# Optimization experiments

Measured on AMD Instinct MI355X. Metric: run time of the kernel, lower is better.

## Reference

```python
import jax, jax.numpy as jnp
import numpy as np
from jax import lax

DN = ('NCHW', 'OIHW', 'NCHW')
MAX_CLAMP = 0.75


def conv_s2(x, w):
    # kernel 9x9, stride 2, padding 4, no bias
    return lax.conv_general_dilated(x, w, window_strides=(2, 2),
                                    padding=[(4, 4), (4, 4)],
                                    dimension_numbers=DN)


def setup_inputs() -> dict:
    key = jax.random.key(0)
    k_x, k1, k2, k3, k4 = jax.random.split(key, 5)
    num_maps = 32
    x = jax.random.normal(k_x, (1024, 2, 128, 128), dtype=jnp.float32)
    # PyTorch Conv2d default init ~ U(-1/sqrt(fan_in), 1/sqrt(fan_in)); scale similarly
    w1 = jax.random.normal(k1, (8, 2, 9, 9), dtype=jnp.float32) * (1.0 / np.sqrt(2 * 81))
    w2 = jax.random.normal(k2, (8, 8, 9, 9), dtype=jnp.float32) * (1.0 / np.sqrt(8 * 81))
    w3 = jax.random.normal(k3, (num_maps, 8, 9, 9), dtype=jnp.float32) * (1.0 / np.sqrt(8 * 81))
    wfc = jax.random.normal(k4, (2, num_maps), dtype=jnp.float32) * (1.0 / np.sqrt(num_maps))
    return {"x": x, "w1": w1, "w2": w2, "w3": w3, "wfc": wfc}


def reference(x, w1, w2, w3, wfc):
    conv1 = jax.nn.relu(conv_s2(x, w1))                  # [B, 8, 64, 64]
    conv2 = jax.nn.relu(conv_s2(conv1, w2))              # [B, 8, 32, 32]
    conv3 = jax.nn.relu(conv_s2(conv2, w3))              # [B, M, 16, 16]
    # per-channel max over 16x16 spatial, threshold at 0.75*max, zero below
    maps_max = jnp.max(conv3, axis=(2, 3), keepdims=True) * MAX_CLAMP
    conv3_masked = jnp.where(conv3 < maps_max, 0.0, conv3)
    pool = jnp.mean(conv3_masked, axis=(2, 3))           # AvgPool2d((16,16)) -> [B, M]
    logits = pool @ wfc.T                                # Linear(M, 2, bias=False)
    y = jax.nn.log_softmax(logits, axis=1)
    return (y, conv3_masked, pool)
```

## Files before the change

### kernel.cpp

```cpp
#include <hip/hip_runtime.h>
#include <hip/hip_bf16.h>
#include <math.h>


#define RELU(v) fmaxf((v), 0.0f)

__device__ __forceinline__ int swzq(int q) { return q ^ ((q >> 3) & 7); }

__global__ __launch_bounds__(256) void conv1_kernel(
    const float* __restrict__ x, const float* __restrict__ w1,
    float* __restrict__ out1) {
  __shared__ float sIn[39 * 164];
  const int tid = threadIdx.x;
  const int b = blockIdx.x >> 2;
  const int oy0 = (blockIdx.x & 3) << 4;
  const int iy0 = 2 * oy0 - 4;
  const float* xb = x + (size_t)b * (2 * 128 * 128);

  const int ty = tid >> 4;
  const int tx = tid & 15;
  int roff[4];
#pragma unroll
  for (int q = 0; q < 4; q++) roff[q] = swzq(2 * tx + q) * 4;

  float acc[8][4];
#pragma unroll
  for (int co = 0; co < 8; co++)
#pragma unroll
    for (int i = 0; i < 4; i++) acc[co][i] = 0.f;

#pragma unroll 1
  for (int ci = 0; ci < 2; ci++) {
    __syncthreads();
    for (int i = tid; i < 39 * 34; i += 256) {
      int r = i / 34;
      int seg = i - r * 34;
      int gy = iy0 + r;
      float4 v = make_float4(0.f, 0.f, 0.f, 0.f);
      if (gy >= 0 && gy < 128 && seg >= 1 && seg <= 32)
        v = *reinterpret_cast<const float4*>(xb + (ci * 128 + gy) * 128 + (seg * 4 - 4));
      *reinterpret_cast<float4*>(&sIn[r * 164 + swzq(seg) * 4]) = v;
    }
    __syncthreads();
#pragma unroll 1
    for (int ky = 0; ky < 9; ky++) {
      const int rb = (2 * ty + ky) * 164;
      float xv[16];
#pragma unroll
      for (int q = 0; q < 4; q++) {
        float4 t = *reinterpret_cast<const float4*>(&sIn[rb + roff[q]]);
        xv[4 * q + 0] = t.x; xv[4 * q + 1] = t.y;
        xv[4 * q + 2] = t.z; xv[4 * q + 3] = t.w;
      }
#pragma unroll
      for (int co = 0; co < 8; co++) {
        const float* wr = w1 + (co * 2 + ci) * 81 + ky * 9;
        float w[9];
#pragma unroll
        for (int k = 0; k < 9; k++) w[k] = wr[k];
#pragma unroll
        for (int kx = 0; kx < 9; kx++)
#pragma unroll
          for (int i = 0; i < 4; i++)
            acc[co][i] = fmaf(xv[kx + 2 * i], w[kx], acc[co][i]);
      }
    }
  }
  const int oy = oy0 + ty;
  float* ob = out1 + (size_t)b * (8 * 64 * 64);
#pragma unroll
  for (int co = 0; co < 8; co++) {
    float4 v = make_float4(RELU(acc[co][0]), RELU(acc[co][1]),
                           RELU(acc[co][2]), RELU(acc[co][3]));
    *reinterpret_cast<float4*>(ob + (co * 64 + oy) * 64 + 4 * tx) = v;
  }
}

__global__ __launch_bounds__(256) void conv2_kernel(
    const float* __restrict__ in, const float* __restrict__ w2,
    float* __restrict__ out2) {
  __shared__ float sIn[71 * 84];
  const int tid = threadIdx.x;
  const int b = blockIdx.x;
  const float* ib = in + (size_t)b * (8 * 64 * 64);
  const int oy = tid >> 3;
  const int tx = tid & 7;
  int roff[4];
#pragma unroll
  for (int q = 0; q < 4; q++) roff[q] = swzq(2 * tx + q) * 4;

  float acc[8][4];
#pragma unroll
  for (int co = 0; co < 8; co++)
#pragma unroll
    for (int i = 0; i < 4; i++) acc[co][i] = 0.f;

#pragma unroll 1
  for (int ci = 0; ci < 8; ci++) {
    __syncthreads();
    for (int i = tid; i < 71 * 18; i += 256) {
      int r = i / 18;
      int seg = i - r * 18;
      int gy = r - 4;
      float4 v = make_float4(0.f, 0.f, 0.f, 0.f);
      if (gy >= 0 && gy < 64 && seg >= 1 && seg <= 16)
        v = *reinterpret_cast<const float4*>(ib + (ci * 64 + gy) * 64 + (seg * 4 - 4));
      *reinterpret_cast<float4*>(&sIn[r * 84 + swzq(seg) * 4]) = v;
    }
    __syncthreads();
#pragma unroll 1
    for (int ky = 0; ky < 9; ky++) {
      const int rb = (2 * oy + ky) * 84;
      float xv[16];
#pragma unroll
      for (int q = 0; q < 4; q++) {
        float4 t = *reinterpret_cast<const float4*>(&sIn[rb + roff[q]]);
        xv[4 * q + 0] = t.x; xv[4 * q + 1] = t.y;
        xv[4 * q + 2] = t.z; xv[4 * q + 3] = t.w;
      }
#pragma unroll
      for (int co = 0; co < 8; co++) {
        const float* wr = w2 + (co * 8 + ci) * 81 + ky * 9;
        float w[9];
#pragma unroll
        for (int k = 0; k < 9; k++) w[k] = wr[k];
#pragma unroll
        for (int kx = 0; kx < 9; kx++)
#pragma unroll
          for (int i = 0; i < 4; i++)
            acc[co][i] = fmaf(xv[kx + 2 * i], w[kx], acc[co][i]);
      }
    }
  }
  float* ob = out2 + (size_t)b * (8 * 32 * 32);
#pragma unroll
  for (int co = 0; co < 8; co++) {
    float4 v = make_float4(RELU(acc[co][0]), RELU(acc[co][1]),
                           RELU(acc[co][2]), RELU(acc[co][3]));
    *reinterpret_cast<float4*>(ob + (co * 32 + oy) * 32 + 4 * tx) = v;
  }
}

__global__ __launch_bounds__(256) void conv3_kernel(
    const float* __restrict__ in, const float* __restrict__ w3,
    float* __restrict__ masked_out, float* __restrict__ pool) {
  __shared__ float sIn[2 * 39 * 44];
  const int tid = threadIdx.x;
  const int b = blockIdx.x;
  const int co0 = __builtin_amdgcn_readfirstlane(tid >> 6) * 8;
  const int p = tid & 63;
  const int oy = p >> 2;
  const int oxg = p & 3;
  const float* ib = in + (size_t)b * (8 * 32 * 32);

  float acc[8][4];
#pragma unroll
  for (int co = 0; co < 8; co++)
#pragma unroll
    for (int i = 0; i < 4; i++) acc[co][i] = 0.f;

#pragma unroll 1
  for (int cg = 0; cg < 4; cg++) {
    __syncthreads();
    for (int i = tid; i < 2 * 39 * 10; i += 256) {
      int c = i / 390;
      int rem = i - c * 390;
      int r = rem / 10;
      int seg = rem - r * 10;
      int gy = r - 4;
      float4 v = make_float4(0.f, 0.f, 0.f, 0.f);
      if (gy >= 0 && gy < 32 && seg >= 1 && seg <= 8)
        v = *reinterpret_cast<const float4*>(ib + ((2 * cg + c) * 32 + gy) * 32 + (seg * 4 - 4));
      *reinterpret_cast<float4*>(&sIn[(c * 39 + r) * 44 + seg * 4]) = v;
    }
    __syncthreads();
#pragma unroll 1
    for (int c = 0; c < 2; c++) {
      const int ci = 2 * cg + c;
#pragma unroll 1
      for (int ky = 0; ky < 9; ky++) {
        const int rb = (c * 39 + 2 * oy + ky) * 44;
        float xv[16];
#pragma unroll
        for (int q = 0; q < 4; q++) {
          float4 t = *reinterpret_cast<const float4*>(&sIn[rb + (2 * oxg + q) * 4]);
          xv[4 * q + 0] = t.x; xv[4 * q + 1] = t.y;
          xv[4 * q + 2] = t.z; xv[4 * q + 3] = t.w;
        }
#pragma unroll
        for (int co = 0; co < 8; co++) {
          const float* wr = w3 + ((co0 + co) * 8 + ci) * 81 + ky * 9;
          float w[9];
#pragma unroll
          for (int k = 0; k < 9; k++) w[k] = wr[k];
#pragma unroll
          for (int kx = 0; kx < 9; kx++)
#pragma unroll
            for (int i = 0; i < 4; i++)
              acc[co][i] = fmaf(xv[kx + 2 * i], w[kx], acc[co][i]);
        }
      }
    }
  }

  float thr[8];
#pragma unroll
  for (int co = 0; co < 8; co++) {
#pragma unroll
    for (int i = 0; i < 4; i++) acc[co][i] = RELU(acc[co][i]);
    float m = fmaxf(fmaxf(acc[co][0], acc[co][1]), fmaxf(acc[co][2], acc[co][3]));
#pragma unroll
    for (int k = 32; k >= 1; k >>= 1) m = fmaxf(m, __shfl_xor(m, k));
    thr[co] = m * 0.75f;
  }

  float* mb = masked_out + ((size_t)b * 32 + co0) * 256 + 4 * p;
  float sum[8];
#pragma unroll
  for (int co = 0; co < 8; co++) {
    float4 v;
    v.x = (acc[co][0] < thr[co]) ? 0.f : acc[co][0];
    v.y = (acc[co][1] < thr[co]) ? 0.f : acc[co][1];
    v.z = (acc[co][2] < thr[co]) ? 0.f : acc[co][2];
    v.w = (acc[co][3] < thr[co]) ? 0.f : acc[co][3];
    *reinterpret_cast<float4*>(mb + co * 256) = v;
    float s = v.x + v.y + v.z + v.w;
#pragma unroll
    for (int k = 32; k >= 1; k >>= 1) s += __shfl_xor(s, k);
    sum[co] = s;
  }
  if (p == 0) {
#pragma unroll
    for (int co = 0; co < 8; co++)
      pool[(size_t)b * 32 + co0 + co] = sum[co] * (1.0f / 256.0f);
  }
}

__global__ __launch_bounds__(256) void head_kernel(
    const float* __restrict__ pool, const float* __restrict__ wfc,
    float* __restrict__ y) {
  __shared__ float sw[64];
  if (threadIdx.x < 64) sw[threadIdx.x] = wfc[threadIdx.x];
  __syncthreads();
  const int b = blockIdx.x * 256 + threadIdx.x;
  const float* pb = pool + (size_t)b * 32;
  float l0 = 0.f, l1 = 0.f;
#pragma unroll
  for (int q = 0; q < 8; q++) {
    float4 p = *reinterpret_cast<const float4*>(pb + 4 * q);
    l0 += p.x * sw[4 * q + 0] + p.y * sw[4 * q + 1] +
          p.z * sw[4 * q + 2] + p.w * sw[4 * q + 3];
    l1 += p.x * sw[32 + 4 * q + 0] + p.y * sw[32 + 4 * q + 1] +
          p.z * sw[32 + 4 * q + 2] + p.w * sw[32 + 4 * q + 3];
  }
  float m = fmaxf(l0, l1);
  float lz = logf(expf(l0 - m) + expf(l1 - m)) + m;
  float2 out = make_float2(l0 - lz, l1 - lz);
  *reinterpret_cast<float2*>(y + 2 * b) = out;
}

extern "C" void kernel_launch(void* const* d_in, const int* in_sizes, int n_in,
                              void* d_out, int out_size, void* d_ws, size_t ws_size,
                              hipStream_t stream) {
  const float* x   = (const float*)d_in[0];
  const float* w1  = (const float*)d_in[1];
  const float* w2  = (const float*)d_in[2];
  const float* w3  = (const float*)d_in[3];
  const float* wfc = (const float*)d_in[4];

  float* out = (float*)d_out;
  float* y      = out;
  float* masked = out + 2048;
  float* pool   = out + 2048 + 1024 * 32 * 256;

  float* c1 = (float*)d_ws;
  float* c2 = c1 + (size_t)1024 * 8 * 64 * 64;

  conv1_kernel<<<4096, 256, 0, stream>>>(x, w1, c1);
  conv2_kernel<<<1024, 256, 0, stream>>>(c1, w2, c2);
  conv3_kernel<<<1024, 256, 0, stream>>>(c2, w3, masked, pool);
  head_kernel<<<4, 256, 0, stream>>>(pool, wfc, y);
}
```

Baseline: 517.8 us.

## Prefetch conv tiles into registers, split conv2 blocks, fuse head into conv3

All three conv kernels now load the next input-channel tile from global memory into registers while computing the current one, then write it to shared memory, so load latency overlaps with FMA work. conv2 is split into two blocks per image, each with half the output rows and 2 outputs per thread, which doubles the grid and shrinks shared memory. conv3 pads rows to 64 floats with an XOR swizzle to avoid LDS bank conflicts, and absorbs the linear + log_softmax head, which removes one launch. The cost is more register pressure from the prefetch buffers, and conv2 now does less work per thread with more redundant weight loads.

```diff
diff --git a/kernel.cpp b/kernel.cpp
--- a/kernel.cpp
+++ b/kernel.cpp
@@ -29,19 +29,41 @@
 #pragma unroll
     for (int i = 0; i < 4; i++) acc[co][i] = 0.f;
 
-#pragma unroll 1
-  for (int ci = 0; ci < 2; ci++) {
-    __syncthreads();
-    for (int i = tid; i < 39 * 34; i += 256) {
-      int r = i / 34;
-      int seg = i - r * 34;
+  float4 pre[6];
+  auto issue = [&](int ci) {
+#pragma unroll
+    for (int k = 0; k < 5; k++) {
+      int idx = tid + 256 * k;
+      int r = idx >> 5, seg = idx & 31;
       int gy = iy0 + r;
       float4 v = make_float4(0.f, 0.f, 0.f, 0.f);
-      if (gy >= 0 && gy < 128 && seg >= 1 && seg <= 32)
+      if (idx < 1248 && gy >= 0 && gy < 128 && seg >= 1)
         v = *reinterpret_cast<const float4*>(xb + (ci * 128 + gy) * 128 + (seg * 4 - 4));
-      *reinterpret_cast<float4*>(&sIn[r * 164 + swzq(seg) * 4]) = v;
-    }
-    __syncthreads();
+      pre[k] = v;
+    }
+    {
+      int r = tid >> 1, seg = 32 + (tid & 1);
+      int gy = iy0 + r;
+      float4 v = make_float4(0.f, 0.f, 0.f, 0.f);
+      if (tid < 78 && gy >= 0 && gy < 128 && seg == 32)
+        v = *reinterpret_cast<const float4*>(xb + (ci * 128 + gy) * 128 + (seg * 4 - 4));
+      pre[5] = v;
+    }
+  };
+  auto wrlds = [&]() {
+#pragma unroll
+    for (int k = 0; k < 5; k++) {
+      int idx = tid + 256 * k;
+      int r = idx >> 5, seg = idx & 31;
+      if (idx < 1248)
+        *reinterpret_cast<float4*>(&sIn[r * 164 + swzq(seg) * 4]) = pre[k];
+    }
+    if (tid < 78) {
+      int r = tid >> 1, seg = 32 + (tid & 1);
+      *reinterpret_cast<float4*>(&sIn[r * 164 + swzq(seg) * 4]) = pre[5];
+    }
+  };
+  auto compute = [&](int ci) {
 #pragma unroll 1
     for (int ky = 0; ky < 9; ky++) {
       const int rb = (2 * ty + ky) * 164;
@@ -65,7 +87,14 @@
             acc[co][i] = fmaf(xv[kx + 2 * i], w[kx], acc[co][i]);
       }
     }
-  }
+  };
+
+  issue(0); wrlds(); __syncthreads();
+  issue(1);
+  compute(0);
+  __syncthreads(); wrlds(); __syncthreads();
+  compute(1);
+
   const int oy = oy0 + ty;
   float* ob = out1 + (size_t)b * (8 * 64 * 64);
 #pragma unroll
@@ -79,41 +108,63 @@
 __global__ __launch_bounds__(256) void conv2_kernel(
     const float* __restrict__ in, const float* __restrict__ w2,
     float* __restrict__ out2) {
-  __shared__ float sIn[71 * 84];
+  __shared__ float sIn[39 * 84];
   const int tid = threadIdx.x;
-  const int b = blockIdx.x;
+  const int b = blockIdx.x >> 1;
+  const int oy0 = (blockIdx.x & 1) << 4;
+  const int gy0 = 2 * oy0 - 4;
   const float* ib = in + (size_t)b * (8 * 64 * 64);
-  const int oy = tid >> 3;
-  const int tx = tid & 7;
-  int roff[4];
-#pragma unroll
-  for (int q = 0; q < 4; q++) roff[q] = swzq(2 * tx + q) * 4;
-
-  float acc[8][4];
-#pragma unroll
-  for (int co = 0; co < 8; co++)
-#pragma unroll
-    for (int i = 0; i < 4; i++) acc[co][i] = 0.f;
-
-#pragma unroll 1
-  for (int ci = 0; ci < 8; ci++) {
-    __syncthreads();
-    for (int i = tid; i < 71 * 18; i += 256) {
-      int r = i / 18;
-      int seg = i - r * 18;
-      int gy = r - 4;
-      float4 v = make_float4(0.f, 0.f, 0.f, 0.f);
-      if (gy >= 0 && gy < 64 && seg >= 1 && seg <= 16)
+  const int oy = tid >> 4;
+  const int tx = tid & 15;
+  int roff[3];
+#pragma unroll
+  for (int q = 0; q < 3; q++) roff[q] = swzq(tx + q) * 4;
+
+  float acc[8][2];
+#pragma unroll
+  for (int co = 0; co < 8; co++) { acc[co][0] = 0.f; acc[co][1] = 0.f; }
+
+  float4 pre[4];
+  auto issue = [&](int ci) {
+#pragma unroll
+    for (int k = 0; k < 3; k++) {
+      int idx = tid + 256 * k;
+      int r = idx >> 4, seg = idx & 15;
+      int gy = gy0 + r;
+      float4 v = make_float4(0.f, 0.f, 0.f, 0.f);
+      if (idx < 624 && gy >= 0 && gy < 64 && seg >= 1)
         v = *reinterpret_cast<const float4*>(ib + (ci * 64 + gy) * 64 + (seg * 4 - 4));
-      *reinterpret_cast<float4*>(&sIn[r * 84 + swzq(seg) * 4]) = v;
-    }
-    __syncthreads();
+      pre[k] = v;
+    }
+    {
+      int r = tid >> 1, seg = 16 + (tid & 1);
+      int gy = gy0 + r;
+      float4 v = make_float4(0.f, 0.f, 0.f, 0.f);
+      if (tid < 78 && gy >= 0 && gy < 64 && seg == 16)
+        v = *reinterpret_cast<const float4*>(ib + (ci * 64 + gy) * 64 + (seg * 4 - 4));
+      pre[3] = v;
+    }
+  };
+  auto wrlds = [&]() {
+#pragma unroll
+    for (int k = 0; k < 3; k++) {
+      int idx = tid + 256 * k;
+      int r = idx >> 4, seg = idx & 15;
+      if (idx < 624)
+        *reinterpret_cast<float4*>(&sIn[r * 84 + swzq(seg) * 4]) = pre[k];
+    }
+    if (tid < 78) {
+      int r = tid >> 1, seg = 16 + (tid & 1);
+      *reinterpret_cast<float4*>(&sIn[r * 84 + swzq(seg) * 4]) = pre[3];
+    }
+  };
+  auto compute = [&](int ci) {
 #pragma unroll 1
     for (int ky = 0; ky < 9; ky++) {
       const int rb = (2 * oy + ky) * 84;
-      float xv[16];
-#pragma unroll
-      for (int q = 0; q < 4; q++) {
+      float xv[12];
+#pragma unroll
+      for (int q = 0; q < 3; q++) {
         float4 t = *reinterpret_cast<const float4*>(&sIn[rb + roff[q]]);
         xv[4 * q + 0] = t.x; xv[4 * q + 1] = t.y;
         xv[4 * q + 2] = t.z; xv[4 * q + 3] = t.w;
@@ -125,26 +176,38 @@
 #pragma unroll
         for (int k = 0; k < 9; k++) w[k] = wr[k];
 #pragma unroll
-        for (int kx = 0; kx < 9; kx++)
-#pragma unroll
-          for (int i = 0; i < 4; i++)
-            acc[co][i] = fmaf(xv[kx + 2 * i], w[kx], acc[co][i]);
-      }
-    }
-  }
+        for (int kx = 0; kx < 9; kx++) {
+          acc[co][0] = fmaf(xv[kx], w[kx], acc[co][0]);
+          acc[co][1] = fmaf(xv[kx + 2], w[kx], acc[co][1]);
+        }
+      }
+    }
+  };
+
+  issue(0); wrlds(); __syncthreads();
+#pragma unroll 1
+  for (int ci = 0; ci < 8; ci++) {
+    if (ci < 7) issue(ci + 1);
+    compute(ci);
+    __syncthreads();
+    if (ci < 7) { wrlds(); __syncthreads(); }
+  }
+
   float* ob = out2 + (size_t)b * (8 * 32 * 32);
+  const int oyg = oy0 + oy;
 #pragma unroll
   for (int co = 0; co < 8; co++) {
-    float4 v = make_float4(RELU(acc[co][0]), RELU(acc[co][1]),
-                           RELU(acc[co][2]), RELU(acc[co][3]));
-    *reinterpret_cast<float4*>(ob + (co * 32 + oy) * 32 + 4 * tx) = v;
+    float2 v = make_float2(RELU(acc[co][0]), RELU(acc[co][1]));
+    *reinterpret_cast<float2*>(ob + (co * 32 + oyg) * 32 + 2 * tx) = v;
   }
 }
 
 __global__ __launch_bounds__(256) void conv3_kernel(
     const float* __restrict__ in, const float* __restrict__ w3,
-    float* __restrict__ masked_out, float* __restrict__ pool) {
-  __shared__ float sIn[2 * 39 * 44];
+    const float* __restrict__ wfc, float* __restrict__ masked_out,
+    float* __restrict__ pool, float* __restrict__ y) {
+  __shared__ float sIn[2 * 39 * 64];
+  __shared__ float sPool[32];
   const int tid = threadIdx.x;
   const int b = blockIdx.x;
   const int co0 = __builtin_amdgcn_readfirstlane(tid >> 6) * 8;
@@ -159,31 +222,61 @@
 #pragma unroll
     for (int i = 0; i < 4; i++) acc[co][i] = 0.f;
 
-#pragma unroll 1
-  for (int cg = 0; cg < 4; cg++) {
-    __syncthreads();
-    for (int i = tid; i < 2 * 39 * 10; i += 256) {
-      int c = i / 390;
-      int rem = i - c * 390;
-      int r = rem / 10;
-      int seg = rem - r * 10;
+  float4 pre[4];
+  auto issue = [&](int cg) {
+#pragma unroll
+    for (int k = 0; k < 3; k++) {
+      int idx = tid + 256 * k;
+      int cr = idx >> 3, seg = idx & 7;
+      int c = (cr >= 39) ? 1 : 0;
+      int r = cr - 39 * c;
       int gy = r - 4;
       float4 v = make_float4(0.f, 0.f, 0.f, 0.f);
-      if (gy >= 0 && gy < 32 && seg >= 1 && seg <= 8)
+      if (idx < 624 && gy >= 0 && gy < 32 && seg >= 1)
         v = *reinterpret_cast<const float4*>(ib + ((2 * cg + c) * 32 + gy) * 32 + (seg * 4 - 4));
-      *reinterpret_cast<float4*>(&sIn[(c * 39 + r) * 44 + seg * 4]) = v;
-    }
-    __syncthreads();
+      pre[k] = v;
+    }
+    {
+      int cr = tid >> 1, seg = 8 + (tid & 1);
+      int c = (cr >= 39) ? 1 : 0;
+      int r = cr - 39 * c;
+      int gy = r - 4;
+      float4 v = make_float4(0.f, 0.f, 0.f, 0.f);
+      if (tid < 156 && gy >= 0 && gy < 32 && seg == 8)
+        v = *reinterpret_cast<const float4*>(ib + ((2 * cg + c) * 32 + gy) * 32 + (seg * 4 - 4));
+      pre[3] = v;
+    }
+  };
+  auto wrlds = [&]() {
+#pragma unroll
+    for (int k = 0; k < 3; k++) {
+      int idx = tid + 256 * k;
+      int cr = idx >> 3, seg = idx & 7;
+      if (idx < 624) {
+        int slot = seg ^ ((cr >> 1) & 7);
+        *reinterpret_cast<float4*>(&sIn[cr * 64 + slot * 4]) = pre[k];
+      }
+    }
+    if (tid < 156) {
+      int cr = tid >> 1, seg = 8 + (tid & 1);
+      int slot = seg ^ ((cr >> 1) & 7);
+      *reinterpret_cast<float4*>(&sIn[cr * 64 + slot * 4]) = pre[3];
+    }
+  };
+  auto compute = [&](int cg) {
 #pragma unroll 1
     for (int c = 0; c < 2; c++) {
       const int ci = 2 * cg + c;
 #pragma unroll 1
       for (int ky = 0; ky < 9; ky++) {
-        const int rb = (c * 39 + 2 * oy + ky) * 44;
+        const int row = c * 39 + 2 * oy + ky;
+        const int rb = row * 64;
+        const int key = (row >> 1) & 7;
         float xv[16];
 #pragma unroll
         for (int q = 0; q < 4; q++) {
-          float4 t = *reinterpret_cast<const float4*>(&sIn[rb + (2 * oxg + q) * 4]);
+          int slot = (2 * oxg + q) ^ key;
+          float4 t = *reinterpret_cast<const float4*>(&sIn[rb + slot * 4]);
           xv[4 * q + 0] = t.x; xv[4 * q + 1] = t.y;
           xv[4 * q + 2] = t.z; xv[4 * q + 3] = t.w;
         }
@@ -201,6 +294,15 @@
         }
       }
     }
+  };
+
+  issue(0); wrlds(); __syncthreads();
+#pragma unroll 1
+  for (int cg = 0; cg < 4; cg++) {
+    if (cg < 3) issue(cg + 1);
+    compute(cg);
+    __syncthreads();
+    if (cg < 3) { wrlds(); __syncthreads(); }
   }
 
   float thr[8];
@@ -231,32 +333,30 @@
   }
   if (p == 0) {
 #pragma unroll
-    for (int co = 0; co < 8; co++)
-      pool[(size_t)b * 32 + co0 + co] = sum[co] * (1.0f / 256.0f);
-  }
-}
-
-__global__ __launch_bounds__(256) void head_kernel(
-    const float* __restrict__ pool, const float* __restrict__ wfc,
-    float* __restrict__ y) {
-  __shared__ float sw[64];
-  if (threadIdx.x < 64) sw[threadIdx.x] = wfc[threadIdx.x];
+    for (int co = 0; co < 8; co++) {
+      float pv = sum[co] * (1.0f / 256.0f);
+      pool[(size_t)b * 32 + co0 + co] = pv;
+      sPool[co0 + co] = pv;
+    }
+  }
   __syncthreads();
-  const int b = blockIdx.x * 256 + threadIdx.x;
-  const float* pb = pool + (size_t)b * 32;
-  float l0 = 0.f, l1 = 0.f;
-#pragma unroll
-  for (int q = 0; q < 8; q++) {
-    float4 p = *reinterpret_cast<const float4*>(pb + 4 * q);
-    l0 += p.x * sw[4 * q + 0] + p.y * sw[4 * q + 1] +
-          p.z * sw[4 * q + 2] + p.w * sw[4 * q + 3];
-    l1 += p.x * sw[32 + 4 * q + 0] + p.y * sw[32 + 4 * q + 1] +
-          p.z * sw[32 + 4 * q + 2] + p.w * sw[32 + 4 * q + 3];
-  }
-  float m = fmaxf(l0, l1);
-  float lz = logf(expf(l0 - m) + expf(l1 - m)) + m;
-  float2 out = make_float2(l0 - lz, l1 - lz);
-  *reinterpret_cast<float2*>(y + 2 * b) = out;
+
+  if (tid < 32) {
+    float pv = sPool[tid];
+    float l0 = pv * wfc[tid];
+    float l1 = pv * wfc[32 + tid];
+#pragma unroll
+    for (int k = 16; k >= 1; k >>= 1) {
+      l0 += __shfl_xor(l0, k);
+      l1 += __shfl_xor(l1, k);
+    }
+    if (tid == 0) {
+      float m = fmaxf(l0, l1);
+      float lz = logf(expf(l0 - m) + expf(l1 - m)) + m;
+      float2 out = make_float2(l0 - lz, l1 - lz);
+      *reinterpret_cast<float2*>(y + 2 * b) = out;
+    }
+  }
 }
 
 extern "C" void kernel_launch(void* const* d_in, const int* in_sizes, int n_in,
@@ -277,7 +377,6 @@
   float* c2 = c1 + (size_t)1024 * 8 * 64 * 64;
 
   conv1_kernel<<<4096, 256, 0, stream>>>(x, w1, c1);
-  conv2_kernel<<<1024, 256, 0, stream>>>(c1, w2, c2);
-  conv3_kernel<<<1024, 256, 0, stream>>>(c2, w3, masked, pool);
-  head_kernel<<<4, 256, 0, stream>>>(pool, wfc, y);
+  conv2_kernel<<<2048, 256, 0, stream>>>(c1, w2, c2);
+  conv3_kernel<<<1024, 256, 0, stream>>>(c2, w3, wfc, masked, pool, y);
 }
```

Measured after the change: 515.9 us. Within noise of the previous version (-0.4%).
